# Kernel tuning notes

Hardware: AMD Instinct MI355X
Metric: run time of the kernel (lower is better)

The kernel has to match this reference:

```python
import jax, jax.numpy as jnp
import numpy as np

N, D, A, K, E = 8192, 256, 1024, 65, 4096

def setup_inputs() -> dict:
    key = jax.random.key(0)
    ks = jax.random.split(key, 8)
    s = 0.02  # linear-init scale to keep activations sane
    return {
        "embedding": jax.random.normal(ks[0], (N, D), jnp.float32),
        "data": jax.random.randint(ks[1], (E, 2), 0, N, jnp.int64),
        "Wq": jax.random.normal(ks[2], (D, A), jnp.float32) * s,
        "bq": jnp.zeros((A,), jnp.float32),
        "Wk": jax.random.normal(ks[3], (D, A), jnp.float32) * s,
        "bk": jnp.zeros((A,), jnp.float32),
        "Wv": jax.random.normal(ks[4], (D, A), jnp.float32) * s,
        "bv": jnp.zeros((A,), jnp.float32),
        "W_edge": jax.random.normal(ks[5], (K, A, A), jnp.float32) * s,
    }

def reference(embedding, data, Wq, bq, Wk, bk, Wv, bv, W_edge):
    # NodeSelfAttention: dense full attention over all N nodes
    Q = embedding @ Wq + bq            # [N, A]
    Km = embedding @ Wk + bk           # [N, A]
    V = embedding @ Wv + bv            # [N, A]
    scale = 1.0 / jnp.sqrt(jnp.float32(D))  # note: sqrt(num_feats)=sqrt(256), as in source
    scores = (Q @ Km.T) * scale        # [N, N]
    attn = jax.nn.softmax(scores, axis=-1)
    attn_emb = attn @ V                # [N, A]
    # gather edge endpoints
    h_u = attn_emb[data[:, 0]]         # [E, A]
    h_v = attn_emb[data[:, 1]]         # [E, A]
    # KWayPred: out[e,k] = h_u[e] @ W_edge[k] @ h_v[e]
    # (source computes full ExE matmul per k and takes diag; this is the
    #  equivalent O(E*K*A^2) bilinear-diag form)
    t = jnp.einsum('ed,kdf->ekf', h_u, W_edge)   # [E, K, A]
    out = jnp.einsum('ekf,ef->ek', t, h_v)       # [E, K]
    return out
```

## Files before the change

kernel.cpp:

```cpp
#include <hip/hip_runtime.h>
#include <cstdio>
#include <cstdint>

#define NTOK 8192
#define DIM  256
#define AA   1024
#define KE   65
#define EE   4096

typedef unsigned short u16;
typedef __attribute__((ext_vector_type(4))) float   f32x4;
typedef __attribute__((ext_vector_type(8))) short   bf16x8;
typedef __attribute__((ext_vector_type(8))) unsigned short u16x8;

#define DEVI __device__ __forceinline__

DEVI u16 f2bf(float f) {
  union { float f; unsigned u; } x; x.f = f;
  unsigned r = x.u + 0x7FFFu + ((x.u >> 16) & 1u);
  return (u16)(r >> 16);
}
DEVI float bf2f(u16 h) {
  union { unsigned u; float f; } x; x.u = ((unsigned)h) << 16;
  return x.f;
}

DEVI void gload16(const void* g, void* l) {
  __builtin_amdgcn_global_load_lds(
      (const __attribute__((address_space(1))) void*)g,
      (__attribute__((address_space(3))) void*)l,
      16, 0, 0);
}

DEVI void barx() {
  asm volatile("" ::: "memory");
  __builtin_amdgcn_s_barrier();
  asm volatile("" ::: "memory");
}

DEVI void stage_half(const u16* __restrict__ g0, int ld, char* dst, int tid) {
#pragma unroll
  for (int rr = 0; rr < 2; ++rr) {
    int o = rr * 8192 + (tid >> 6) * 1024 + (tid & 63) * 16;
    int q = o ^ (((o >> 7) & 7) << 4);
    gload16(g0 + (size_t)(q >> 7) * ld + ((q & 127) >> 1),
            dst + rr * 8192 + (tid >> 6) * 1024);
  }
}

DEVI void stage_t4(const u16* __restrict__ g0, int ld, char* dst, int tid) {
#pragma unroll
  for (int rr = 0; rr < 4; ++rr) {
    int o = rr * 4096 + tid * 16;
    int q = o ^ (((o >> 7) & 7) << 4);
    gload16(g0 + (size_t)(q >> 7) * ld + ((q & 127) >> 1),
            dst + rr * 4096 + (tid >> 6) * 1024);
  }
}

template<int EPI, int QMODE>
__global__ __launch_bounds__(256, 2)
void gemm4(const u16* __restrict__ A, int lda,
           const u16* __restrict__ B, int ldb,
           int MT, int NT, int K,
           u16* __restrict__ o_s, float scale, int ldc,
           const u16* __restrict__ Hu, float* __restrict__ o_e,
           int* __restrict__ qcnt)
{
  __shared__ __align__(16) char lds[65536];
  __shared__ int s_idx;
  char* ldsA = lds;
  char* ldsB = lds + 32768;

  const int tid = threadIdx.x, lane = tid & 63, wave = tid >> 6;
  const int wm = (wave >> 1) * 64, wn = (wave & 1) * 64;
  const int KT = K >> 6;
  const int r15 = lane & 15, g16 = (lane >> 4) << 4;

  int xcc;
  asm volatile("s_getreg_b32 %0, hwreg(20, 0, 32)" : "=s"(xcc));
  xcc &= 7;
  const int MPX = MT >> 3;
  const int NQ = NT >> 3, NR = NT & 7;

  for (int dx = 0; dx < 8; ++dx) {
    const int qi = (xcc + dx) & 7;
    int per, ntb = 0, ntc = 0;
    if constexpr (QMODE == 0) {
      per = (MT * NT) >> 3;
    } else {
      ntc = NQ + (qi < NR ? 1 : 0);
      ntb = qi * NQ + (qi < NR ? qi : NR);
      per = ntc * MT;
    }
    while (true) {
      if (tid == 0) s_idx = atomicAdd(&qcnt[qi], 1);
      __syncthreads();
      const int idx = s_idx;
      __syncthreads();
      if (idx >= per) break;
      int mt, nt;
      if constexpr (QMODE == 0) {
        mt = qi * MPX + (idx % MPX); nt = idx / MPX;
      } else {
        const int srw = ntc << 3;
        const int sr = idx / srw, rem = idx - sr * srw;
        nt = ntb + (rem >> 3); mt = (sr << 3) + (rem & 7);
      }
      const int m0 = mt * 128, n0 = nt * 128;
      const u16* Ag = A + (size_t)m0 * lda;
      const u16* Bg = B + (size_t)n0 * ldb;

      f32x4 acc[4][4];
#pragma unroll
      for (int m = 0; m < 4; ++m)
#pragma unroll
        for (int n = 0; n < 4; ++n) acc[m][n] = f32x4{0.f, 0.f, 0.f, 0.f};

      stage_t4(Ag,      lda, ldsA,         tid);
      stage_t4(Bg,      ldb, ldsB,         tid);
      stage_t4(Ag + 64, lda, ldsA + 16384, tid);
      stage_t4(Bg + 64, ldb, ldsB + 16384, tid);
      asm volatile("s_waitcnt vmcnt(8)" ::: "memory");
      barx();

      for (int t = 0; t < KT; ++t) {
        const char* Ab = ldsA + (t & 1) * 16384;
        const char* Bb = ldsB + (t & 1) * 16384;
        bf16x8 a[4][2], b[4][2];
#pragma unroll
        for (int m = 0; m < 4; ++m)
#pragma unroll
          for (int kk = 0; kk < 2; ++kk) {
            int p = (wm + m * 16 + r15) * 128 + kk * 64 + g16;
            p ^= ((p >> 7) & 7) << 4;
            a[m][kk] = *(const bf16x8*)(Ab + p);
          }
#pragma unroll
        for (int n = 0; n < 4; ++n)
#pragma unroll
          for (int kk = 0; kk < 2; ++kk) {
            int p = (wn + n * 16 + r15) * 128 + kk * 64 + g16;
            p ^= ((p >> 7) & 7) << 4;
            b[n][kk] = *(const bf16x8*)(Bb + p);
          }
        asm volatile("s_waitcnt lgkmcnt(0)" ::: "memory");
        __builtin_amdgcn_sched_barrier(0);
        barx();
        if (t + 2 < KT) {
          stage_t4(Ag + (size_t)(t + 2) * 64, lda, ldsA + (t & 1) * 16384, tid);
          stage_t4(Bg + (size_t)(t + 2) * 64, ldb, ldsB + (t & 1) * 16384, tid);
        }
        __builtin_amdgcn_s_setprio(1);
#pragma unroll
        for (int kk = 0; kk < 2; ++kk)
#pragma unroll
          for (int m = 0; m < 4; ++m)
#pragma unroll
            for (int n = 0; n < 4; ++n)
              acc[m][n] = __builtin_amdgcn_mfma_f32_16x16x32_bf16(
                  a[m][kk], b[n][kk], acc[m][n], 0, 0, 0);
        __builtin_amdgcn_s_setprio(0);
        if (t + 2 < KT) asm volatile("s_waitcnt vmcnt(8)" ::: "memory");
        else            asm volatile("s_waitcnt vmcnt(0)" ::: "memory");
        barx();
      }

      const int rgrp = lane >> 4, cid = lane & 15;
      if constexpr (EPI == 1) {
#pragma unroll
        for (int m = 0; m < 4; ++m)
#pragma unroll
          for (int n = 0; n < 4; ++n)
#pragma unroll
            for (int j = 0; j < 4; ++j) {
              int row = m0 + wm + m * 16 + rgrp * 4 + j;
              int col = n0 + wn + n * 16 + cid;
              o_s[(size_t)row * ldc + col] = f2bf(acc[m][n][j] * scale);
            }
      } else {
        const int kidx  = n0 >> 10;
        const int dbase = (n0 & 1023) + wn;
#pragma unroll
        for (int m = 0; m < 4; ++m)
#pragma unroll
          for (int j = 0; j < 4; ++j) {
            int row = m0 + wm + m * 16 + rgrp * 4 + j;
            float p = 0.f;
#pragma unroll
            for (int n = 0; n < 4; ++n)
              p += acc[m][n][j] * bf2f(Hu[(size_t)row * AA + dbase + n * 16 + cid]);
            p += __shfl_xor(p, 1, 64);
            p += __shfl_xor(p, 2, 64);
            p += __shfl_xor(p, 4, 64);
            p += __shfl_xor(p, 8, 64);
            if (cid == 0) atomicAdd(&o_e[(size_t)row * KE + kidx], p);
          }
      }
    }
  }
}

template<int EPI, int QMODE>
__global__ __launch_bounds__(512, 2)
void gemm8(const u16* __restrict__ A, int lda,
           const u16* __restrict__ B, int ldb,
           int MT, int NT, int K,
           u16* __restrict__ o_s, float scale, int ldc,
           const u16* __restrict__ Hu, float* __restrict__ o_e,
           int* __restrict__ qcnt)
{
  __shared__ __align__(16) char lds[131072];
  __shared__ int s_next[3];
  char* ldsA = lds;
  char* ldsB = lds + 65536;

  const int tid = threadIdx.x, lane = tid & 63, wave = tid >> 6;
  const int wm = (wave >> 2) * 128;
  const int wn = (wave & 3) * 64;
  const int wnl = (wave & 1) * 64;
  const int KT = K >> 6, KT2 = KT >> 1;
  const int r15 = lane & 15, g16 = (lane >> 4) << 4;

  int xcc;
  asm volatile("s_getreg_b32 %0, hwreg(20, 0, 32)" : "=s"(xcc));
  xcc &= 7;
  const int MPX = MT >> 3;
  const int NQ = NT >> 3, NR = NT & 7;

  const char* Ab_e = ldsA +         (wm >> 7) * 16384;
  const char* Ab_o = ldsA + 32768 + (wm >> 7) * 16384;
  const char* Bb_e = ldsB +         (wn >> 7) * 16384;
  const char* Bb_o = ldsB + 32768 + (wn >> 7) * 16384;

  int dxr = 0;
  auto pop_next = [&]() {
    while (dxr < 8) {
      const int qi = (xcc + dxr) & 7;
      int per, ntb = 0, ntc = 0;
      if constexpr (QMODE == 0) {
        per = (MT * NT) >> 3;
      } else {
        ntc = NQ + (qi < NR ? 1 : 0);
        ntb = qi * NQ + (qi < NR ? qi : NR);
        per = ntc * MT;
      }
      const int idx = atomicAdd(&qcnt[qi], 1);
      if (idx < per) {
        int mt, nt;
        if constexpr (QMODE == 0) {
          mt = qi * MPX + (idx % MPX); nt = idx / MPX;
        } else {
          const int srw = ntc << 3;
          const int sr = idx / srw, rem = idx - sr * srw;
          nt = ntb + (rem >> 3); mt = (sr << 3) + (rem & 7);
        }
        s_next[0] = mt * 256; s_next[1] = nt * 256; s_next[2] = 1;
        return;
      }
      ++dxr;
    }
    s_next[2] = 0;
  };

  if (tid == 0) pop_next();
  __syncthreads();
  int m0 = s_next[0], n0 = s_next[1];
  if (!s_next[2]) return;

#define STAGE_A2(tk, h) do { const int _tk = (tk); \
    if (_tk < KT) stage_half(A + (size_t)(m0 + (h)*128) * lda + (size_t)_tk*64, lda, \
                             ldsA + (_tk & 1) * 32768 + (h) * 16384, tid); \
    else if (have_n) stage_half(A + (size_t)(m0n + (h)*128) * lda + (size_t)(_tk-KT)*64, lda, \
                                ldsA + (_tk & 1) * 32768 + (h) * 16384, tid); } while (0)
#define STAGE_B2(tk, h) do { const int _tk = (tk); \
    if (_tk < KT) stage_half(B + (size_t)(n0 + (h)*128) * ldb + (size_t)_tk*64, ldb, \
                             ldsB + (_tk & 1) * 32768 + (h) * 16384, tid); \
    else if (have_n) stage_half(B + (size_t)(n0n + (h)*128) * ldb + (size_t)(_tk-KT)*64, ldb, \
                                ldsB + (_tk & 1) * 32768 + (h) * 16384, tid); } while (0)
#define RD_A4(base, q) \
  _Pragma("unroll") for (int m = (q)*4; m < (q)*4+4; ++m) \
  _Pragma("unroll") for (int kk = 0; kk < 2; ++kk) { \
    int p = (m*16 + r15)*128 + kk*64 + g16; p ^= ((p>>7)&7)<<4; \
    a[m][kk] = *(const bf16x8*)((base) + p); }
#define RD_B2(base, q) \
  _Pragma("unroll") for (int n = (q)*2; n < (q)*2+2; ++n) \
  _Pragma("unroll") for (int kk = 0; kk < 2; ++kk) { \
    int p = (wnl + n*16 + r15)*128 + kk*64 + g16; p ^= ((p>>7)&7)<<4; \
    b[n][kk] = *(const bf16x8*)((base) + p); }
#define MM(QM, QN) do { \
  __builtin_amdgcn_s_setprio(1); \
  _Pragma("unroll") for (int kk = 0; kk < 2; ++kk) \
  _Pragma("unroll") for (int m = 0; m < 4; ++m) \
  _Pragma("unroll") for (int n = 0; n < 2; ++n) \
    acc[(QM)*4+m][(QN)*2+n] = __builtin_amdgcn_mfma_f32_16x16x32_bf16( \
        a[(QM)*4+m][kk], b[(QN)*2+n][kk], acc[(QM)*4+m][(QN)*2+n], 0, 0, 0); \
  __builtin_amdgcn_s_setprio(0); } while (0)
#define WAIT_LGKM0 do { asm volatile("s_waitcnt lgkmcnt(0)" ::: "memory"); \
                        __builtin_amdgcn_sched_barrier(0); } while (0)
#define KTILE(t, AB, BB) do { \
    RD_B2(BB, 0); RD_A4(AB, 0); \
    STAGE_B2((t) + 1, 1); \
    asm volatile("s_waitcnt lgkmcnt(8)" ::: "memory"); \
    barx(); WAIT_LGKM0; \
    MM(0, 0); \
    barx(); \
    RD_B2(BB, 1); \
    barx(); WAIT_LGKM0; \
    MM(0, 1); \
    barx(); \
    RD_A4(AB, 1); \
    STAGE_B2((t) + 2, 0); \
    barx(); WAIT_LGKM0; \
    MM(1, 1); \
    barx(); \
    STAGE_A2((t) + 2, 0); \
    STAGE_A2((t) + 2, 1); \
    barx(); \
    __builtin_amdgcn_sched_barrier(0); \
    MM(1, 0); \
    if (vm6) asm volatile("s_waitcnt vmcnt(6)" ::: "memory"); \
    else     asm volatile("s_waitcnt vmcnt(0)" ::: "memory"); \
    barx(); } while (0)

  {
    const int m0n = 0, n0n = 0; const bool have_n = false; (void)m0n; (void)n0n; (void)have_n;
    STAGE_A2(0, 0); STAGE_A2(0, 1); STAGE_B2(0, 0); STAGE_B2(0, 1);
    STAGE_B2(1, 0); STAGE_A2(1, 0); STAGE_A2(1, 1);
  }
  asm volatile("s_waitcnt vmcnt(6)" ::: "memory");
  barx();

  while (true) {
    f32x4 acc[8][4];
#pragma unroll
    for (int m = 0; m < 8; ++m)
#pragma unroll
      for (int n = 0; n < 4; ++n) acc[m][n] = f32x4{0.f, 0.f, 0.f, 0.f};

    int m0n = 0, n0n = 0;
    bool have_n = false;

    for (int i = 0; i < KT2; ++i) {
      const int ta = 2 * i, tb = 2 * i + 1;
      if (i == KT2 - 2 && tid == 0) pop_next();
      if (i == KT2 - 1) { m0n = s_next[0]; n0n = s_next[1]; have_n = (s_next[2] != 0); }
      const bool tail = (i == KT2 - 1);
      const bool vm6 = !tail || have_n;
      bf16x8 a[8][2], b[4][2];
      KTILE(ta, Ab_e, Bb_e);
      KTILE(tb, Ab_o, Bb_o);
    }

    const int rgrp = lane >> 4, cid = lane & 15;
    if constexpr (EPI == 1) {
#pragma unroll
      for (int m = 0; m < 8; ++m)
#pragma unroll
        for (int n = 0; n < 4; ++n)
#pragma unroll
          for (int j = 0; j < 4; ++j) {
            int row = m0 + wm + m * 16 + rgrp * 4 + j;
            int col = n0 + wn + n * 16 + cid;
            o_s[(size_t)row * ldc + col] = f2bf(acc[m][n][j] * scale);
          }
    } else {
      const int kidx  = n0 >> 10;
      const int dbase = (n0 & 1023) + wn;
#pragma unroll
      for (int m = 0; m < 8; ++m)
#pragma unroll
        for (int j = 0; j < 4; ++j) {
          int row = m0 + wm + m * 16 + rgrp * 4 + j;
          float p = 0.f;
#pragma unroll
          for (int n = 0; n < 4; ++n)
            p += acc[m][n][j] * bf2f(Hu[(size_t)row * AA + dbase + n * 16 + cid]);
          p += __shfl_xor(p, 1, 64);
          p += __shfl_xor(p, 2, 64);
          p += __shfl_xor(p, 4, 64);
          p += __shfl_xor(p, 8, 64);
          if (cid == 0) atomicAdd(&o_e[(size_t)row * KE + kidx], p);
        }
    }

    if (!have_n) break;
    m0 = m0n; n0 = n0n;
  }
#undef STAGE_A2
#undef STAGE_B2
#undef RD_A4
#undef RD_B2
#undef MM
#undef WAIT_LGKM0
#undef KTILE
}

#define BM 128
#define BN 128
#define BK 64

template<int EPI, bool BF32>
__global__ __launch_bounds__(256)
void gemm_bt(const u16* __restrict__ A, int lda,
             const void* __restrict__ Bptr, int ldb,
             int MT, int NT, int K,
             u16* __restrict__ o_q, u16* __restrict__ o_k, u16* __restrict__ o_vt,
             const float* __restrict__ biasc,
             u16* __restrict__ o_s, float scale, int ldc,
             const u16* __restrict__ Hu, float* __restrict__ o_e)
{
  const int nb  = MT * NT;
  const int per = nb >> 3;
  int bid = blockIdx.x;
  bid = (bid & 7) * per + (bid >> 3);
  const int mt = bid % MT, nt = bid / MT;
  const int m0 = mt * BM, n0 = nt * BN;

  __shared__ u16 As[BM * BK];
  __shared__ u16 Bs[BN * BK];

  const int tid  = threadIdx.x;
  const int lane = tid & 63, wave = tid >> 6;
  const int wm = (wave >> 1) * 64, wn = (wave & 1) * 64;

  f32x4 acc[4][4];
#pragma unroll
  for (int m = 0; m < 4; ++m)
#pragma unroll
    for (int n = 0; n < 4; ++n) acc[m][n] = f32x4{0.f, 0.f, 0.f, 0.f};

  const u16*   Bh = (const u16*)Bptr;
  const float* Bf = (const float*)Bptr;

  const int KT = K / BK;
  for (int kt = 0; kt < KT; ++kt) {
    const int k0 = kt * BK;
#pragma unroll
    for (int it = 0; it < 4; ++it) {
      int o = it * 4096 + wave * 1024 + lane * 16;
      int r = o >> 7;
      int c = (o & 127) >> 1;
      gload16(A + (size_t)(m0 + r) * lda + k0 + c,
              &As[(it * 4096 + wave * 1024) >> 1]);
    }
    if constexpr (!BF32) {
#pragma unroll
      for (int it = 0; it < 4; ++it) {
        int o = it * 4096 + wave * 1024 + lane * 16;
        int r = o >> 7;
        int c = (o & 127) >> 1;
        gload16(Bh + (size_t)(n0 + r) * ldb + k0 + c,
                &Bs[(it * 4096 + wave * 1024) >> 1]);
      }
    } else {
#pragma unroll
      for (int it = 0; it < 8; ++it) {
        int e = it * 1024 + tid * 4;
        int r = e >> 6, c = e & 63;
        const float4 v = *(const float4*)(Bf + (size_t)(n0 + r) * ldb + k0 + c);
        ushort4 h;
        h.x = f2bf(v.x); h.y = f2bf(v.y); h.z = f2bf(v.z); h.w = f2bf(v.w);
        *(ushort4*)&Bs[r * BK + c] = h;
      }
    }
    asm volatile("s_waitcnt vmcnt(0)" ::: "memory");
    __syncthreads();

#pragma unroll
    for (int kk = 0; kk < 2; ++kk) {
      const int ro = lane & 15;
      const int ko = kk * 32 + (lane >> 4) * 8;
      bf16x8 af[4], bfg[4];
#pragma unroll
      for (int m = 0; m < 4; ++m)
        af[m] = *(const bf16x8*)&As[(wm + m * 16 + ro) * BK + ko];
#pragma unroll
      for (int n = 0; n < 4; ++n)
        bfg[n] = *(const bf16x8*)&Bs[(wn + n * 16 + ro) * BK + ko];
#pragma unroll
      for (int m = 0; m < 4; ++m)
#pragma unroll
        for (int n = 0; n < 4; ++n)
          acc[m][n] = __builtin_amdgcn_mfma_f32_16x16x32_bf16(
              af[m], bfg[n], acc[m][n], 0, 0, 0);
    }
    __syncthreads();
  }

  const int rgrp = lane >> 4, cid = lane & 15;

  if constexpr (EPI == 0) {
#pragma unroll
    for (int m = 0; m < 4; ++m)
#pragma unroll
      for (int n = 0; n < 4; ++n)
#pragma unroll
        for (int j = 0; j < 4; ++j) {
          int row = m0 + wm + m * 16 + rgrp * 4 + j;
          int col = n0 + wn + n * 16 + cid;
          float v = acc[m][n][j] + biasc[col];
          u16 h = f2bf(v);
          if (col < 1024)       o_q[(size_t)row * AA + col] = h;
          else if (col < 2048)  o_k[(size_t)row * AA + (col - 1024)] = h;
          else                  o_vt[(size_t)(col - 2048) * NTOK + row] = h;
        }
  } else if constexpr (EPI == 1) {
#pragma unroll
    for (int m = 0; m < 4; ++m)
#pragma unroll
      for (int n = 0; n < 4; ++n)
#pragma unroll
        for (int j = 0; j < 4; ++j) {
          int row = m0 + wm + m * 16 + rgrp * 4 + j;
          int col = n0 + wn + n * 16 + cid;
          o_s[(size_t)row * ldc + col] = f2bf(acc[m][n][j] * scale);
        }
  } else {
    const int kidx  = n0 >> 10;
    const int dbase = (n0 & 1023) + wn;
#pragma unroll
    for (int m = 0; m < 4; ++m)
#pragma unroll
      for (int j = 0; j < 4; ++j) {
        int row = m0 + wm + m * 16 + rgrp * 4 + j;
        float p = 0.f;
#pragma unroll
        for (int n = 0; n < 4; ++n) {
          int d = dbase + n * 16 + cid;
          p += acc[m][n][j] * bf2f(Hu[(size_t)row * AA + d]);
        }
        p += __shfl_xor(p, 1, 64);
        p += __shfl_xor(p, 2, 64);
        p += __shfl_xor(p, 4, 64);
        p += __shfl_xor(p, 8, 64);
        if (cid == 0) atomicAdd(&o_e[(size_t)row * KE + kidx], p);
      }
  }
}

__global__ __launch_bounds__(256)
void softmax_rows(u16* __restrict__ S)
{
  const size_t base = (size_t)blockIdx.x * 8192;
  const int tid = threadIdx.x;
  const int lane = tid & 63, wave = tid >> 6;
  float v[32];
#pragma unroll
  for (int c = 0; c < 4; ++c) {
    u16x8 u = *(const u16x8*)&S[base + c * 2048 + tid * 8];
#pragma unroll
    for (int j = 0; j < 8; ++j) v[c * 8 + j] = bf2f(u[j]);
  }
  float mx = -1e30f;
#pragma unroll
  for (int i = 0; i < 32; ++i) mx = fmaxf(mx, v[i]);
#pragma unroll
  for (int off = 1; off < 64; off <<= 1) mx = fmaxf(mx, __shfl_xor(mx, off, 64));
  __shared__ float r1[4], r2[4];
  if (lane == 0) r1[wave] = mx;
  __syncthreads();
  mx = fmaxf(fmaxf(r1[0], r1[1]), fmaxf(r1[2], r1[3]));

  float s = 0.f;
#pragma unroll
  for (int i = 0; i < 32; ++i) { v[i] = __expf(v[i] - mx); s += v[i]; }
#pragma unroll
  for (int off = 1; off < 64; off <<= 1) s += __shfl_xor(s, off, 64);
  if (lane == 0) r2[wave] = s;
  __syncthreads();
  s = r2[0] + r2[1] + r2[2] + r2[3];
  const float inv = 1.f / s;
#pragma unroll
  for (int c = 0; c < 4; ++c) {
    u16x8 u;
#pragma unroll
    for (int j = 0; j < 8; ++j) u[j] = f2bf(v[c * 8 + j] * inv);
    *(u16x8*)&S[base + c * 2048 + tid * 8] = u;
  }
}

__global__ __launch_bounds__(256)
void gather_rows(const unsigned* __restrict__ dw, const u16* __restrict__ AE,
                 u16* __restrict__ Hu, u16* __restrict__ Hv)
{
  bool i64 = true;
#pragma unroll
  for (int w = 1; w < 32; w += 2) i64 = i64 && (dw[w] == 0u);
  const int e = blockIdx.x;
  const unsigned iu = i64 ? dw[4 * e]     : dw[2 * e];
  const unsigned iv = i64 ? dw[4 * e + 2] : dw[2 * e + 1];
  const int t = threadIdx.x;
  *(ushort4*)&Hu[(size_t)e * AA + t * 4] = *(const ushort4*)&AE[(size_t)iu * AA + t * 4];
  *(ushort4*)&Hv[(size_t)e * AA + t * 4] = *(const ushort4*)&AE[(size_t)iv * AA + t * 4];
}

__global__ __launch_bounds__(256)
void init_misc(float* __restrict__ out_e, const float* __restrict__ bq,
               const float* __restrict__ bk, const float* __restrict__ bv,
               float* __restrict__ biasc, int* __restrict__ qall)
{
  const int i = blockIdx.x * 256 + threadIdx.x;
  if (i < EE * KE) out_e[i] = 0.f;
  if (i < 1024) {
    biasc[i]        = bq[i];
    biasc[1024 + i] = bk[i];
    biasc[2048 + i] = bv[i];
  }
  if (i < 64) qall[i] = 0;
}

__global__ __launch_bounds__(256)
void cvt_f32_bf16_v4(const float* __restrict__ src, u16* __restrict__ dst, int n4)
{
  for (int i = blockIdx.x * 256 + threadIdx.x; i < n4; i += gridDim.x * 256) {
    float4 v = ((const float4*)src)[i];
    ushort4 h; h.x = f2bf(v.x); h.y = f2bf(v.y); h.z = f2bf(v.z); h.w = f2bf(v.w);
    ((ushort4*)dst)[i] = h;
  }
}

__global__ __launch_bounds__(256)
void build_wT(const float* __restrict__ Wq, const float* __restrict__ Wk,
              const float* __restrict__ Wv, u16* __restrict__ WT)
{
  const int nn = blockIdx.x;
  const int d  = threadIdx.x;
  const float* W = (nn < 1024) ? Wq : ((nn < 2048) ? Wk : Wv);
  WT[nn * DIM + d] = f2bf(W[(size_t)d * AA + (nn & 1023)]);
}

extern "C" void kernel_launch(void* const* d_in, const int* in_sizes, int n_in,
                              void* d_out, int out_size, void* d_ws, size_t ws_size,
                              hipStream_t stream)
{
  (void)in_sizes; (void)out_size;
  if (n_in < 9) return;
  const float*    emb  = (const float*)d_in[0];
  const unsigned* data = (const unsigned*)d_in[1];
  const float* Wq = (const float*)d_in[2];
  const float* bq = (const float*)d_in[3];
  const float* Wk = (const float*)d_in[4];
  const float* bk = (const float*)d_in[5];
  const float* Wv = (const float*)d_in[6];
  const float* bv = (const float*)d_in[7];
  const float* We = (const float*)d_in[8];
  float* out = (float*)d_out;

  char* ws = (char*)d_ws;
  size_t off = 0;
  auto alloc = [&](size_t bytes) -> void* {
    void* p = ws + off;
    off += (bytes + 255) & ~(size_t)255;
    return p;
  };
  u16*   emb_b = (u16*)alloc((size_t)NTOK * DIM * 2);
  u16*   WT    = (u16*)alloc((size_t)3072 * DIM * 2);
  float* biasc = (float*)alloc(3072 * 4);
  int*   qall  = (int*)alloc(64 * 4);
  u16*   Qb    = (u16*)alloc((size_t)NTOK * AA * 2);
  u16*   Kb    = (u16*)alloc((size_t)NTOK * AA * 2);
  u16*   Vt    = (u16*)alloc((size_t)AA * NTOK * 2);
  u16*   AE    = (u16*)alloc((size_t)NTOK * AA * 2);
  u16*   Hu    = (u16*)alloc((size_t)EE * AA * 2);
  u16*   Hv    = (u16*)alloc((size_t)EE * AA * 2);

  const size_t webf_bytes = ((size_t)KE * AA * AA * 2 + 255) & ~(size_t)255;
  u16* We_b = nullptr;
  if (off + webf_bytes + (size_t)1024 * NTOK * 2 <= ws_size) {
    We_b = (u16*)(ws + off);
    off += webf_bytes;
  }

  int chunk = 4096;
  while (chunk > 128 && off + (size_t)chunk * NTOK * 2 > ws_size) chunk >>= 1;
  u16* Sc = (u16*)alloc((size_t)chunk * NTOK * 2);
  if (off > ws_size) {
    fprintf(stderr, "kernel_launch: ws too small (need %zu, have %zu)\n", off, ws_size);
    return;
  }

  init_misc<<<(EE * KE) / 256, 256, 0, stream>>>(out, bq, bk, bv, biasc, qall);
  cvt_f32_bf16_v4<<<2048, 256, 0, stream>>>(emb, emb_b, NTOK * DIM / 4);
  build_wT<<<3072, 256, 0, stream>>>(Wq, Wk, Wv, WT);
  if (We_b)
    cvt_f32_bf16_v4<<<4096, 256, 0, stream>>>(We, We_b, KE * AA * AA / 4);

  gemm_bt<0, false><<<64 * 24, 256, 0, stream>>>(
      emb_b, DIM, WT, DIM, 64, 24, DIM,
      Qb, Kb, Vt, biasc, nullptr, 0.f, 0, nullptr, nullptr);

  const int nch = NTOK / chunk;
  for (int ci = 0; ci < nch; ++ci) {
    const u16* Qc = Qb + (size_t)ci * chunk * AA;
    const bool big = ((chunk & 2047) == 0);
    if (big)
      gemm8<1, 1><<<256, 512, 0, stream>>>(
          Qc, AA, Kb, AA, chunk / 256, 32, AA,
          Sc, 0.0625f, NTOK, nullptr, nullptr, qall + 8 * ci);
    else
      gemm_bt<1, false><<<(chunk / 128) * 64, 256, 0, stream>>>(
          Qc, AA, Kb, AA, chunk / 128, 64, AA,
          nullptr, nullptr, nullptr, nullptr, Sc, 0.0625f, NTOK, nullptr, nullptr);
    softmax_rows<<<chunk, 256, 0, stream>>>(Sc);
    gemm_bt<1, false><<<(chunk / 128) * 8, 256, 0, stream>>>(
        Sc, NTOK, Vt, NTOK, chunk / 128, 8, NTOK,
        nullptr, nullptr, nullptr, nullptr,
        AE + (size_t)ci * chunk * AA, 1.0f, AA, nullptr, nullptr);
  }

  gather_rows<<<EE, 256, 0, stream>>>(data, AE, Hu, Hv);

  if (We_b)
    gemm4<2, 1><<<512, 256, 0, stream>>>(
        Hv, AA, We_b, AA, 32, 520, AA,
        nullptr, 0.f, 0, Hu, out, qall + 32);
  else
    gemm_bt<3, true><<<32 * 520, 256, 0, stream>>>(
        Hv, AA, We, AA, 32, 520, AA,
        nullptr, nullptr, nullptr, nullptr, nullptr, 0.f, 0, Hu, out);
}
```

Measured before the change: 1.518 ms.

## Use triple-buffered 32-wide K tiles in persistent GEMM and apply to attn@V

Restructures the persistent gemm4 kernel into gemm4t with a K-step of 32 instead of 64, three LDS stages at 8 KB per operand instead of two 16 KB stages, and a prefetch distance of three. LDS per block falls to 48 KB, so launch bounds allow three blocks per CU and the grids grow to 768. The attn@V GEMM for large chunks now also uses this queue-based kernel instead of gemm_bt. In exchange there are more barriers per unit of work and less MFMA work between them.

```diff
diff --git a/kernel.cpp b/kernel.cpp
--- a/kernel.cpp
+++ b/kernel.cpp
@@ -48,34 +48,34 @@
   }
 }
 
-DEVI void stage_t4(const u16* __restrict__ g0, int ld, char* dst, int tid) {
-#pragma unroll
-  for (int rr = 0; rr < 4; ++rr) {
+DEVI void stage_t32(const u16* __restrict__ g0, int ld, char* dst, int tid) {
+#pragma unroll
+  for (int rr = 0; rr < 2; ++rr) {
     int o = rr * 4096 + tid * 16;
-    int q = o ^ (((o >> 7) & 7) << 4);
-    gload16(g0 + (size_t)(q >> 7) * ld + ((q & 127) >> 1),
+    int q = o ^ (((o >> 7) & 3) << 4);
+    gload16(g0 + (size_t)(q >> 6) * ld + ((q & 63) >> 1),
             dst + rr * 4096 + (tid >> 6) * 1024);
   }
 }
 
 template<int EPI, int QMODE>
-__global__ __launch_bounds__(256, 2)
-void gemm4(const u16* __restrict__ A, int lda,
-           const u16* __restrict__ B, int ldb,
-           int MT, int NT, int K,
-           u16* __restrict__ o_s, float scale, int ldc,
-           const u16* __restrict__ Hu, float* __restrict__ o_e,
-           int* __restrict__ qcnt)
-{
-  __shared__ __align__(16) char lds[65536];
+__global__ __launch_bounds__(256, 3)
+void gemm4t(const u16* __restrict__ A, int lda,
+            const u16* __restrict__ B, int ldb,
+            int MT, int NT, int K,
+            u16* __restrict__ o_s, float scale, int ldc,
+            const u16* __restrict__ Hu, float* __restrict__ o_e,
+            int* __restrict__ qcnt)
+{
+  __shared__ __align__(16) char lds[49152];
   __shared__ int s_idx;
   char* ldsA = lds;
-  char* ldsB = lds + 32768;
+  char* ldsB = lds + 24576;
 
   const int tid = threadIdx.x, lane = tid & 63, wave = tid >> 6;
   const int wm = (wave >> 1) * 64, wn = (wave & 1) * 64;
-  const int KT = K >> 6;
-  const int r15 = lane & 15, g16 = (lane >> 4) << 4;
+  const int KT = K >> 5;
+  const int r15 = lane & 15, g16b = (lane >> 4) * 16;
 
   int xcc;
   asm volatile("s_getreg_b32 %0, hwreg(20, 0, 32)" : "=s"(xcc));
@@ -117,53 +117,52 @@
 #pragma unroll
         for (int n = 0; n < 4; ++n) acc[m][n] = f32x4{0.f, 0.f, 0.f, 0.f};
 
-      stage_t4(Ag,      lda, ldsA,         tid);
-      stage_t4(Bg,      ldb, ldsB,         tid);
-      stage_t4(Ag + 64, lda, ldsA + 16384, tid);
-      stage_t4(Bg + 64, ldb, ldsB + 16384, tid);
+      stage_t32(Ag,      lda, ldsA,         tid);
+      stage_t32(Bg,      ldb, ldsB,         tid);
+      stage_t32(Ag + 32, lda, ldsA + 8192,  tid);
+      stage_t32(Bg + 32, ldb, ldsB + 8192,  tid);
+      stage_t32(Ag + 64, lda, ldsA + 16384, tid);
+      stage_t32(Bg + 64, ldb, ldsB + 16384, tid);
       asm volatile("s_waitcnt vmcnt(8)" ::: "memory");
       barx();
 
+      int bi = 0;
       for (int t = 0; t < KT; ++t) {
-        const char* Ab = ldsA + (t & 1) * 16384;
-        const char* Bb = ldsB + (t & 1) * 16384;
-        bf16x8 a[4][2], b[4][2];
-#pragma unroll
-        for (int m = 0; m < 4; ++m)
-#pragma unroll
-          for (int kk = 0; kk < 2; ++kk) {
-            int p = (wm + m * 16 + r15) * 128 + kk * 64 + g16;
-            p ^= ((p >> 7) & 7) << 4;
-            a[m][kk] = *(const bf16x8*)(Ab + p);
-          }
-#pragma unroll
-        for (int n = 0; n < 4; ++n)
-#pragma unroll
-          for (int kk = 0; kk < 2; ++kk) {
-            int p = (wn + n * 16 + r15) * 128 + kk * 64 + g16;
-            p ^= ((p >> 7) & 7) << 4;
-            b[n][kk] = *(const bf16x8*)(Bb + p);
-          }
+        const char* Ab = ldsA + bi * 8192;
+        const char* Bb = ldsB + bi * 8192;
+        bf16x8 a[4], b[4];
+#pragma unroll
+        for (int m = 0; m < 4; ++m) {
+          int p = (wm + m * 16 + r15) * 64 + g16b;
+          p ^= ((p >> 7) & 3) << 4;
+          a[m] = *(const bf16x8*)(Ab + p);
+        }
+#pragma unroll
+        for (int n = 0; n < 4; ++n) {
+          int p = (wn + n * 16 + r15) * 64 + g16b;
+          p ^= ((p >> 7) & 3) << 4;
+          b[n] = *(const bf16x8*)(Bb + p);
+        }
         asm volatile("s_waitcnt lgkmcnt(0)" ::: "memory");
         __builtin_amdgcn_sched_barrier(0);
         barx();
-        if (t + 2 < KT) {
-          stage_t4(Ag + (size_t)(t + 2) * 64, lda, ldsA + (t & 1) * 16384, tid);
-          stage_t4(Bg + (size_t)(t + 2) * 64, ldb, ldsB + (t & 1) * 16384, tid);
+        if (t + 3 < KT) {
+          stage_t32(Ag + (size_t)(t + 3) * 32, lda, ldsA + bi * 8192, tid);
+          stage_t32(Bg + (size_t)(t + 3) * 32, ldb, ldsB + bi * 8192, tid);
         }
         __builtin_amdgcn_s_setprio(1);
 #pragma unroll
-        for (int kk = 0; kk < 2; ++kk)
-#pragma unroll
-          for (int m = 0; m < 4; ++m)
-#pragma unroll
-            for (int n = 0; n < 4; ++n)
-              acc[m][n] = __builtin_amdgcn_mfma_f32_16x16x32_bf16(
-                  a[m][kk], b[n][kk], acc[m][n], 0, 0, 0);
+        for (int m = 0; m < 4; ++m)
+#pragma unroll
+          for (int n = 0; n < 4; ++n)
+            acc[m][n] = __builtin_amdgcn_mfma_f32_16x16x32_bf16(
+                a[m], b[n], acc[m][n], 0, 0, 0);
         __builtin_amdgcn_s_setprio(0);
-        if (t + 2 < KT) asm volatile("s_waitcnt vmcnt(8)" ::: "memory");
-        else            asm volatile("s_waitcnt vmcnt(0)" ::: "memory");
+        if (t + 3 < KT)      asm volatile("s_waitcnt vmcnt(8)" ::: "memory");
+        else if (t + 2 < KT) asm volatile("s_waitcnt vmcnt(4)" ::: "memory");
+        else                 asm volatile("s_waitcnt vmcnt(0)" ::: "memory");
         barx();
+        bi = (bi == 2) ? 0 : bi + 1;
       }
 
       const int rgrp = lane >> 4, cid = lane & 15;
@@ -703,16 +702,22 @@
           Qc, AA, Kb, AA, chunk / 128, 64, AA,
           nullptr, nullptr, nullptr, nullptr, Sc, 0.0625f, NTOK, nullptr, nullptr);
     softmax_rows<<<chunk, 256, 0, stream>>>(Sc);
-    gemm_bt<1, false><<<(chunk / 128) * 8, 256, 0, stream>>>(
-        Sc, NTOK, Vt, NTOK, chunk / 128, 8, NTOK,
-        nullptr, nullptr, nullptr, nullptr,
-        AE + (size_t)ci * chunk * AA, 1.0f, AA, nullptr, nullptr);
+    if (big)
+      gemm4t<1, 1><<<768, 256, 0, stream>>>(
+          Sc, NTOK, Vt, NTOK, chunk / 128, 8, NTOK,
+          AE + (size_t)ci * chunk * AA, 1.0f, AA, nullptr, nullptr,
+          qall + 16 + 8 * ci);
+    else
+      gemm_bt<1, false><<<(chunk / 128) * 8, 256, 0, stream>>>(
+          Sc, NTOK, Vt, NTOK, chunk / 128, 8, NTOK,
+          nullptr, nullptr, nullptr, nullptr,
+          AE + (size_t)ci * chunk * AA, 1.0f, AA, nullptr, nullptr);
   }
 
   gather_rows<<<EE, 256, 0, stream>>>(data, AE, Hu, Hv);
 
   if (We_b)
-    gemm4<2, 1><<<512, 256, 0, stream>>>(
+    gemm4t<2, 1><<<768, 256, 0, stream>>>(
         Hv, AA, We_b, AA, 32, 520, AA,
         nullptr, 0.f, 0, Hu, out, qall + 32);
   else
```

New measurement: 1.579 ms. +4.0%, slower.
